# Kernel optimization log

Measured on AMD Instinct MI355X. Metric: run time of the kernel, lower is better.

The kernel has to match this reference:

```python
import jax, jax.numpy as jnp
import numpy as np

B, T, D = 64, 64, 64
E, HA, HB, OUT = 128, 128, 128, 1
SHORT = 2


def _rn(k, shape, scale=0.05):
    return jax.random.normal(k, shape, dtype=jnp.float32) * scale


def setup_inputs() -> dict:
    key = jax.random.key(0)
    ks = jax.random.split(key, 18)
    return {
        "x": jax.random.normal(ks[0], (B, T, D), dtype=jnp.float32),
        "W_emb": _rn(ks[1], (E, D)), "b_emb": _rn(ks[2], (E,)),
        "Wi_a": _rn(ks[3], (3 * HA, E)), "Wh_a": _rn(ks[4], (3 * HA, HA)),
        "bi_a": _rn(ks[5], (3 * HA,)), "bh_a": _rn(ks[6], (3 * HA,)),
        "Wi_b": _rn(ks[7], (3 * HB, E)), "Wh_b": _rn(ks[8], (3 * HB, HB)),
        "bi_b": _rn(ks[9], (3 * HB,)), "bh_b": _rn(ks[10], (3 * HB,)),
        "Wa": _rn(ks[11], (1, HA)), "ba": _rn(ks[12], (1,)),
        "Wb": _rn(ks[13], (E, HB)), "bb": _rn(ks[14], (E,)),
        "Wo": _rn(ks[15], (OUT, E)), "bo": _rn(ks[16], (OUT,)),
        "short": SHORT,
    }


def _gru_cell(x, h, Wi, Wh, bi, bh):
    # PyTorch GRU cell: gates ordered (r, z, n)
    gi = x @ Wi.T + bi
    gh = h @ Wh.T + bh
    ir, iz, in_ = jnp.split(gi, 3, axis=-1)
    hr, hz, hn = jnp.split(gh, 3, axis=-1)
    r = jax.nn.sigmoid(ir + hr)
    z = jax.nn.sigmoid(iz + hz)
    n = jnp.tanh(in_ + r * hn)
    return (1.0 - z) * n + z * h


def _forward(x, W_emb, b_emb, Wi_a, Wh_a, bi_a, bh_a, Wi_b, Wh_b, bi_b, bh_b,
             Wa, ba, Wb, bb, Wo, bo, short):
    Bn, Tn = x.shape[0], x.shape[1]
    temp = jnp.transpose(x, (1, 0, 2))            # [T, B, D]
    emb = temp @ W_emb.T + b_emb                  # [T, B, E]
    P = Tn - 1                                    # prefix p handles att_timesteps t = p+1
    S = Tn - 1                                    # max reversed-prefix length
    p_idx = jnp.arange(P)
    h0a = jnp.zeros((P, Bn, Wh_a.shape[1]), x.dtype)
    h0b = jnp.zeros((P, Bn, Wh_b.shape[1]), x.dtype)

    # All prefixes at once: for prefix p, reversed input at step s is emb[p - s].
    def step(carry, s):
        ha, hb = carry
        j = jnp.clip(p_idx - s, 0, Tn - 1)        # [P]
        e_in = emb[j]                             # [P, B, E]
        x_in = temp[j]                            # [P, B, D]
        na = _gru_cell(e_in, ha, Wi_a, Wh_a, bi_a, bh_a)
        nb = _gru_cell(e_in, hb, Wi_b, Wh_b, bi_b, bh_b)
        valid = (p_idx >= s)[:, None, None]
        ha = jnp.where(valid, na, ha)
        hb = jnp.where(valid, nb, hb)
        return (ha, hb), (ha, hb, e_in, x_in)

    _, (Ha, Hb, Eg, Xg) = jax.lax.scan(step, (h0a, h0b), jnp.arange(S))
    Ha = 0.5 * Ha                                 # reverse_h_a * 0.5, [S, P, B, HA]
    Hb = 0.5 * Hb                                 # reverse_h_b * 0.5, [S, P, B, HB]

    mask = p_idx[None, :] >= jnp.arange(S)[:, None]   # [S, P] valid scan steps
    preA = jnp.einsum('spbh,h->spb', Ha, Wa[0]) + ba[0]
    preA = jnp.where(mask[:, :, None], preA, -jnp.inf)
    alpha = jax.nn.softmax(preA, axis=0)              # softmax over prefix positions
    beta = jnp.tanh(jnp.einsum('spbh,eh->spbe', Hb, Wb) + bb)  # [S, P, B, E]

    # context: c[p] = sum_s alpha * beta * emb[p-s]  (softmax is order-invariant)
    c = jnp.einsum('spb,spbe->pbe', alpha, beta * Eg)          # [P, B, E]
    pred = c @ Wo.T + bo                                        # [P, B, 1]

    # interpretability weights: e = (beta * w_out) @ W_emb, f = alpha*e*x, g = mean over prefix
    e_chain = jnp.einsum('spbe,ed->spbd', beta * Wo[0], W_emb)  # [S, P, B, D]
    f = alpha[..., None] * e_chain * Xg
    g = jnp.sum(f, axis=0) / (p_idx[:, None, None] + 1.0)       # mean over t = p+1 steps

    pred = jnp.transpose(pred[short + 1:], (1, 0, 2))           # [B, T-2-short, 1]
    weight = jnp.transpose(g[short + 1:], (1, 0, 2))            # [B, T-2-short, D]
    return pred, weight


def reference(x, W_emb, b_emb, Wi_a, Wh_a, bi_a, bh_a, Wi_b, Wh_b, bi_b, bh_b,
              Wa, ba, Wb, bb, Wo, bo, short):
    return _forward(x, W_emb, b_emb, Wi_a, Wh_a, bi_a, bh_a, Wi_b, Wh_b, bi_b,
                    bh_b, Wa, ba, Wb, bb, Wo, bo, short)
```

## Files before the change

### kernel.cpp

```cpp
#include <hip/hip_runtime.h>
#include <hip/hip_bf16.h>
#include <math.h>

#define B_ 64
#define T_ 64
#define D_ 64
#define PMIN 3
#define NPOUT 60
#define NCHUNK 4

#define LOG2E     1.4426950408889634f
#define TWOLOG2E  2.8853900817779268f

typedef __hip_bfloat16 bf16;
typedef __attribute__((ext_vector_type(4))) short s16x4;
typedef __attribute__((ext_vector_type(8))) short s16x8;
typedef __attribute__((ext_vector_type(4))) float f32x4;

#define OFF_EMB   0
#define OFF_WIC2  524288
#define OFF_XT    622592
#define OFF_GIPK  884736
#define OFF_WPK   2457600
#define OFF_BPPK  2506752
#define OFF_WMPK  2514944
#define OFF_WALPK 2519040
#define OFF_FLAG  2520064

__device__ __forceinline__ float bf2f(unsigned short u) {
    union { float f; unsigned u32; } x; x.u32 = ((unsigned)u) << 16; return x.f;
}
__device__ __forceinline__ unsigned short f2bf(float f) {
    union { float f; unsigned u; } x; x.f = f;
    unsigned r = x.u + 0x7FFFu + ((x.u >> 16) & 1u);
    return (unsigned short)(r >> 16);
}
__device__ __forceinline__ float LDF(const void* p, int i, int flag) {
    return flag ? ((const float*)p)[i] : bf2f(((const unsigned short*)p)[i]);
}
__device__ __forceinline__ float sig2(float xneg) {
    return __builtin_amdgcn_rcpf(1.f + __builtin_exp2f(xneg));
}
__device__ __forceinline__ float tanh2(float x2) {
    return 1.f - 2.f * __builtin_amdgcn_rcpf(1.f + __builtin_exp2f(x2));
}
__device__ __forceinline__ int kpi(int s) {
    return (s & ~31) | ((s & 1) << 4) | ((s & 31) >> 1);
}

__global__ void detect_dtype(const unsigned short* xr, int* flag)
{
    int tid = threadIdx.x;
    int bad = 0;
    for (int i = tid; i < 4096; i += 256) {
        int ex = (xr[i] >> 7) & 0xFF;
        if (ex >= 140) bad++;
    }
    __shared__ int s[256];
    s[tid] = bad;
    __syncthreads();
    for (int st = 128; st > 0; st >>= 1) {
        if (tid < st) s[tid] += s[tid + st];
        __syncthreads();
    }
    if (tid == 0) *flag = (s[0] > 4) ? 1 : 0;
}

__global__ void prep_all(const void* p_x, const void* p_wemb,
                         const void* p_wia, const void* p_wib,
                         const void* p_wha, const void* p_whb,
                         const void* p_wa, const void* p_wb, const void* p_wo,
                         float* ws, const int* flagp)
{
    const int flag = *flagp;
    int id = blockIdx.x * 256 + threadIdx.x;
    if (id < 98304) {
        float v = (id < 49152) ? LDF(p_wia, id, flag)
                               : LDF(p_wib, id - 49152, flag);
        ws[OFF_WIC2 + id] = v;
    } else if (id < 360448) {
        int id5 = id - 98304;
        int b = id5 & 63, d = (id5 >> 6) & 63, t = id5 >> 12;
        ws[OFF_XT + id5] = LDF(p_x, (b * 64 + t) * 64 + d, flag);
    } else if (id < 458752) {
        unsigned short* wpk = (unsigned short*)(ws + OFF_WPK);
        int id3 = id - 360448;
        int w = id3 / 12288, r1 = id3 % 12288;
        int nt = r1 / 2048, r2 = r1 % 2048;
        int kt = r2 / 512, r3 = r2 % 512;
        int lane = r3 >> 3, j = r3 & 7;
        int cell = w >> 2, wv = w & 3;
        int gate = nt >> 1, tt = nt & 1;
        int g = gate * 128 + wv * 32 + tt * 16 + (lane & 15);
        int k = kpi(kt * 32 + (lane >> 4) * 8 + j);
        float sc = (gate < 2) ? -LOG2E : TWOLOG2E;
        wpk[id3] = f2bf(sc * LDF(cell ? p_whb : p_wha, g * 128 + k, flag));
    } else if (id < 475136) {
        unsigned short* bpk = (unsigned short*)(ws + OFF_BPPK);
        int id4 = id - 458752;
        int w = id4 / 2048, r = id4 % 2048;
        int kt = r / 512, lane = (r % 512) >> 3, j = r & 7;
        int e = w * 16 + (lane & 15);
        int k = kpi(kt * 32 + (lane >> 4) * 8 + j);
        bpk[id4] = f2bf(LOG2E * LDF(p_wb, e * 128 + k, flag));
    } else if (id < 483328) {
        unsigned short* wmk = (unsigned short*)(ws + OFF_WMPK);
        int id6 = id - 475136;
        int nt = id6 / 2048, r = id6 % 2048;
        int kt = r / 512, lane = (r % 512) >> 3, j = r & 7;
        int d = nt * 16 + (lane & 15);
        int e = kt * 32 + (lane >> 4) * 8 + j;
        wmk[id6] = f2bf(LDF(p_wo, e, flag) * LDF(p_wemb, e * 64 + d, flag));
    } else {
        unsigned short* alk = (unsigned short*)(ws + OFF_WALPK);
        int id7 = id - 483328;
        int kt = id7 / 512, lane = (id7 % 512) >> 3, j = id7 & 7;
        int k = kpi(kt * 32 + (lane >> 4) * 8 + j);
        alk[id7] = ((lane & 15) == 0) ? f2bf(0.5f * LOG2E * LDF(p_wa, k, flag))
                                      : (unsigned short)0;
    }
}

__global__ void prep_gi(float* ws, const void* p_x, const void* p_wemb,
                        const void* p_bemb, const void* p_bia, const void* p_bha,
                        const void* p_bib, const void* p_bhb, const int* flagp)
{
    const int flag = *flagp;
    unsigned short* gipk = (unsigned short*)(ws + OFF_GIPK);
    int t = blockIdx.x >> 3;
    int chunk = blockIdx.x & 7;
    int b0 = chunk * 8;
    int tid = threadIdx.x;
    __shared__ __align__(16) float sX[8][64];
    __shared__ __align__(16) float sWe[128][64];
    __shared__ __align__(16) float semT2[8][132];
    __shared__ __align__(16) unsigned short stg[6144];

    for (int i = tid; i < 512; i += 256) {
        int r = i >> 6, d = i & 63;
        sX[r][d] = LDF(p_x, ((b0 + r) * 64 + t) * 64 + d, flag);
    }
    for (int i = tid; i < 8192; i += 256)
        sWe[i >> 6][i & 63] = LDF(p_wemb, i, flag);
    __syncthreads();

    #pragma unroll
    for (int q = 0; q < 4; q++) {
        int o = tid + q * 256;
        int e = o & 127, r = o >> 7;
        float acc = LDF(p_bemb, e, flag);
        #pragma unroll
        for (int d = 0; d < 64; d += 4) {
            f32x4 xv = *(const f32x4*)&sX[r][d];
            f32x4 wv = *(const f32x4*)&sWe[e][d];
            acc += xv[0]*wv[0] + xv[1]*wv[1] + xv[2]*wv[2] + xv[3]*wv[3];
        }
        semT2[r][e] = acc;
        ws[OFF_EMB + (size_t)((t * 64 + b0 + r) * 128) + e] = acc;
    }
    __syncthreads();

    float acc3[3][8];
    #pragma unroll
    for (int g3 = 0; g3 < 3; g3++)
        #pragma unroll
        for (int r = 0; r < 8; r++) acc3[g3][r] = 0.f;
    const float* w2 = ws + OFF_WIC2;
    #pragma unroll 2
    for (int e0 = 0; e0 < 128; e0 += 4) {
        f32x4 wv0 = *(const f32x4*)(w2 + (size_t)(tid      ) * 128 + e0);
        f32x4 wv1 = *(const f32x4*)(w2 + (size_t)(tid + 256) * 128 + e0);
        f32x4 wv2 = *(const f32x4*)(w2 + (size_t)(tid + 512) * 128 + e0);
        f32x4 h[8];
        #pragma unroll
        for (int r = 0; r < 8; r++) h[r] = *(const f32x4*)&semT2[r][e0];
        #pragma unroll
        for (int r = 0; r < 8; r++)
            #pragma unroll
            for (int c = 0; c < 4; c++) {
                acc3[0][r] += wv0[c] * h[r][c];
                acc3[1][r] += wv1[c] * h[r][c];
                acc3[2][r] += wv2[c] * h[r][c];
            }
    }
    #pragma unroll
    for (int g3 = 0; g3 < 3; g3++) {
        int g = tid + g3 * 256;
        int cellg = g / 384, gr = g % 384;
        int gate = gr / 128, kh = gr % 128;
        int wvp = kh / 32, tt2 = (kh % 32) / 16, l15p = kh % 16;
        int wq = cellg * 4 + wvp;
        float bias = LDF(cellg ? p_bib : p_bia, gr, flag);
        if (gate < 2) bias += LDF(cellg ? p_bhb : p_bha, gr, flag);
        float sc = (gate < 2) ? -LOG2E : TWOLOG2E;
        #pragma unroll
        for (int r = 0; r < 8; r++) {
            float v = sc * (acc3[g3][r] + bias);
            int lane2 = (r >> 2) * 16 + l15p;
            int slot = gate * 8 + tt2 * 4 + (r & 3);
            stg[(wq * 32 + lane2) * 24 + slot] = f2bf(v);
        }
    }
    __syncthreads();
    const uint4* s4 = (const uint4*)stg;
    const int c16 = chunk >> 1, rhalf = chunk & 1;
    uint4* d4 = (uint4*)(gipk + (size_t)(t * 4 + c16) * 12288);
    for (int i = tid; i < 768; i += 256) {
        int wq = i / 96, rem = i % 96;
        d4[wq * 192 + rhalf * 96 + rem] = s4[i];
    }
}


__launch_bounds__(512, 1)
__global__ void chain_kernel(const float* ws, void* outv, const int* flagp,
                             const void* p_bha, const void* p_bhb,
                             const void* p_bb, const void* p_ba,
                             const void* p_bo, const void* p_wo)
{
    const int p = PMIN + (NPOUT - 1) - (int)blockIdx.x / NCHUNK;
    const int chunk = (int)blockIdx.x % NCHUNK;
    const int tid = threadIdx.x;
    const int lane = tid & 63;
    const int w = tid >> 6;
    const int cell = w >> 2;
    const int wv = w & 3;
    const int l15 = lane & 15;
    const int quad = lane >> 4;

    __shared__ __align__(16) short hbf[2][2][16][136];
    __shared__ __align__(16) short betbf[2][16][136];
    __shared__ __align__(16) short sWm[4][4][64][8];
    __shared__ float weLds[2][16];

    const unsigned short* gipk = (const unsigned short*)(ws + OFF_GIPK);
    const unsigned short* wpk  = (const unsigned short*)(ws + OFF_WPK);
    const unsigned short* bpk  = (const unsigned short*)(ws + OFF_BPPK);
    const unsigned short* alk  = (const unsigned short*)(ws + OFF_WALPK);
    const int flag = *flagp;

    {
        const int* s2 = (const int*)(ws + OFF_WMPK);
        int* d2 = (int*)&sWm[0][0][0][0];
        for (int i = tid; i < 4096; i += 512) d2[i] = s2[i];
        int* hz = (int*)&hbf[0][0][0][0];
        for (int i = tid; i < 4352; i += 512) hz[i] = 0;
        int* bz = (int*)&betbf[0][0][0];
        for (int i = tid; i < 2176; i += 512) bz[i] = 0;
    }

    s16x8 wB[6][4];
    #pragma unroll
    for (int nt = 0; nt < 6; nt++)
        #pragma unroll
        for (int kt = 0; kt < 4; kt++)
            wB[nt][kt] = *(const s16x8*)(wpk + (((w * 6 + nt) * 4 + kt) * 64 + lane) * 8);
    s16x8 bBp[4], wAl[4];
    #pragma unroll
    for (int kt = 0; kt < 4; kt++)
        bBp[kt] = *(const s16x8*)(bpk + ((w * 4 + kt) * 64 + lane) * 8);
    if (w == 7) {
        #pragma unroll
        for (int kt = 0; kt < 4; kt++)
            wAl[kt] = *(const s16x8*)(alk + (kt * 64 + lane) * 8);
    }

    const float bhnS0 = TWOLOG2E *
        LDF(cell ? p_bhb : p_bha, 256 + wv * 32 + l15, flag);
    const float bhnS1 = TWOLOG2E *
        LDF(cell ? p_bhb : p_bha, 256 + wv * 32 + 16 + l15, flag);
    const float bbE2 = TWOLOG2E * LDF(p_bb, w * 16 + l15, flag);
    const float bafS = LOG2E * LDF(p_ba, 0, flag);
    const float bof  = LDF(p_bo, 0, flag);

    float h_old[8];
    #pragma unroll
    for (int i = 0; i < 8; i++) h_old[i] = 0.f;
    float accR[9];
    #pragma unroll
    for (int i = 0; i < 9; i++) accR[i] = 0.f;

    f32x4 xvP = (f32x4){0.f,0.f,0.f,0.f};
    f32x4 em0P = (f32x4){0.f,0.f,0.f,0.f};
    f32x4 em1P = (f32x4){0.f,0.f,0.f,0.f};

    auto phaseC = [&](int dbufP) {
        if (w < 4) {
            f32x4 ec = (f32x4){0.f,0.f,0.f,0.f};
            #pragma unroll
            for (int kt = 0; kt < 4; kt++) {
                s16x8 a = *(const s16x8*)&betbf[dbufP][l15][kt * 32 + quad * 8];
                s16x8 bw = *(const s16x8*)&sWm[w][kt][lane][0];
                ec = __builtin_amdgcn_mfma_f32_16x16x32_bf16(a, bw, ec, 0, 0, 0);
            }
            #pragma unroll
            for (int reg = 0; reg < 4; reg++) {
                float we = weLds[dbufP][quad * 4 + reg];
                accR[4 + reg] += we;
                accR[reg] += we * ec[reg] * xvP[reg];
            }
        } else {
            const int row = quad * 4 + (w - 4);
            float we = weLds[dbufP][row];
            accR[8] += we;
            const short* bp2 = &betbf[dbufP][row][l15 * 8];
            s16x4 blo = *(const s16x4*)bp2;
            s16x4 bhi = *(const s16x4*)(bp2 + 4);
            #pragma unroll
            for (int v = 0; v < 4; v++)
                accR[v] += we * bf2f((unsigned short)blo[v]) * em0P[v];
            #pragma unroll
            for (int v = 0; v < 4; v++)
                accR[4 + v] += we * bf2f((unsigned short)bhi[v]) * em1P[v];
        }
    };

    __syncthreads();

    for (int it = 0; it <= p + 1; it++) {
        const int j = p - it;
        const int jp = j + 1;
        const bool doGru = (j >= 0);
        const int cur = it & 1;
        const int nxt = cur ^ 1;
        const int dbuf = it & 1;

        s16x8 giv[3];
        if (doGru) {
            const unsigned short* gp0 =
                gipk + ((((size_t)j * 4 + chunk) * 8 + w) * 64 + lane) * 24;
            giv[0] = *(const s16x8*)(gp0);
            giv[1] = *(const s16x8*)(gp0 + 8);
            giv[2] = *(const s16x8*)(gp0 + 16);
        }

        if (it > 1) phaseC(dbuf ^ 1);

        if (it > 0) {
            if (w < 4) {
                xvP = *(const f32x4*)(ws + OFF_XT + ((size_t)jp * 64 + w * 16 + l15) * 64
                                      + chunk * 16 + quad * 4);
            } else {
                const int row = quad * 4 + (w - 4);
                const float* ep = ws + OFF_EMB
                                  + ((size_t)jp * 64 + chunk * 16 + row) * 128 + l15 * 8;
                em0P = *(const f32x4*)ep;
                em1P = *(const f32x4*)(ep + 4);
            }
        }

        f32x4 Cg[6], Cbp, Cal;
        #pragma unroll
        for (int nt = 0; nt < 6; nt++) Cg[nt] = (f32x4){0.f,0.f,0.f,0.f};
        Cbp = (f32x4){0.f,0.f,0.f,0.f};
        Cal = (f32x4){0.f,0.f,0.f,0.f};

        #pragma unroll
        for (int kt = 0; kt < 4; kt++) {
            s16x8 aB = *(const s16x8*)&hbf[cur][1][l15][kt * 32 + quad * 8];
            s16x8 aA;
            if (cell == 0 || w == 7) aA = *(const s16x8*)&hbf[cur][0][l15][kt * 32 + quad * 8];
            else aA = aB;
            s16x8 aOwn = cell ? aB : aA;
            #pragma unroll
            for (int nt = 0; nt < 6; nt++)
                Cg[nt] = __builtin_amdgcn_mfma_f32_16x16x32_bf16(aOwn, wB[nt][kt], Cg[nt], 0, 0, 0);
            Cbp = __builtin_amdgcn_mfma_f32_16x16x32_bf16(aB, bBp[kt], Cbp, 0, 0, 0);
            if (w == 7)
                Cal = __builtin_amdgcn_mfma_f32_16x16x32_bf16(aA, wAl[kt], Cal, 0, 0, 0);
        }

        if (w == 7 && l15 == 0) {
            #pragma unroll
            for (int reg = 0; reg < 4; reg++)
                weLds[dbuf][quad * 4 + reg] =
                    __builtin_exp2f(fminf(Cal[reg] + bafS, 86.f));
        }
        if (doGru) {
            #pragma unroll
            for (int reg = 0; reg < 4; reg++) {
                float rr0 = sig2(bf2f((unsigned short)giv[0][reg]) + Cg[0][reg]);
                float zz0 = sig2(bf2f((unsigned short)giv[1][reg]) + Cg[2][reg]);
                float nn0 = tanh2(bf2f((unsigned short)giv[2][reg])
                                  + rr0 * (Cg[4][reg] + bhnS0));
                float h0 = (1.f - zz0) * nn0 + zz0 * h_old[reg];
                h_old[reg] = h0;
                float rr1 = sig2(bf2f((unsigned short)giv[0][4 + reg]) + Cg[1][reg]);
                float zz1 = sig2(bf2f((unsigned short)giv[1][4 + reg]) + Cg[3][reg]);
                float nn1 = tanh2(bf2f((unsigned short)giv[2][4 + reg])
                                  + rr1 * (Cg[5][reg] + bhnS1));
                float h1 = (1.f - zz1) * nn1 + zz1 * h_old[4 + reg];
                h_old[4 + reg] = h1;
                unsigned pk;
                asm("v_cvt_pk_bf16_f32 %0, %1, %2" : "=v"(pk) : "v"(h0), "v"(h1));
                *(unsigned*)&hbf[nxt][cell][quad * 4 + reg][wv * 32 + l15 * 2] = pk;
            }
        }
        {
            #pragma unroll
            for (int reg = 0; reg < 4; reg++) {
                float bv = tanh2(Cbp[reg] + bbE2);
                betbf[dbuf][quad * 4 + reg][w * 16 + l15] = (short)f2bf(bv);
            }
        }

        __syncthreads();
    }

    phaseC((p + 1) & 1);

    if (w >= 4) {
        const int row = quad * 4 + (w - 4);
        float wo8[8];
        if (flag) {
            const float* wp = (const float*)p_wo + l15 * 8;
            #pragma unroll
            for (int v = 0; v < 8; v++) wo8[v] = wp[v];
        } else {
            const unsigned short* wp = (const unsigned short*)p_wo + l15 * 8;
            #pragma unroll
            for (int v = 0; v < 8; v++) wo8[v] = bf2f(wp[v]);
        }
        float part = 0.f;
        #pragma unroll
        for (int v = 0; v < 8; v++) part += accR[v] * wo8[v];
        part += __shfl_xor(part, 1);
        part += __shfl_xor(part, 2);
        part += __shfl_xor(part, 4);
        part += __shfl_xor(part, 8);
        if (l15 == 0) {
            int bglob = chunk * 16 + row;
            float pr = part / accR[8] + bof;
            size_t oi = (size_t)bglob * NPOUT + (p - PMIN);
            if (flag) ((float*)outv)[oi] = pr;
            else      ((bf16*)outv)[oi] = __float2bfloat16(pr);
        }
    } else {
        const float invt = 1.f / (float)(p + 1);
        #pragma unroll
        for (int reg = 0; reg < 4; reg++) {
            int row = quad * 4 + reg;
            int bglob = chunk * 16 + row;
            float gv = accR[reg] / accR[4 + reg] * invt;
            size_t oi = (size_t)B_ * NPOUT
                      + ((size_t)bglob * NPOUT + (p - PMIN)) * 64 + w * 16 + l15;
            if (flag) ((float*)outv)[oi] = gv;
            else      ((bf16*)outv)[oi] = __float2bfloat16(gv);
        }
    }
}

extern "C" void kernel_launch(void* const* d_in, const int* in_sizes, int n_in,
                              void* d_out, int out_size, void* d_ws, size_t ws_size,
                              hipStream_t stream)
{
    float* ws = (float*)d_ws;
    int* flagp = (int*)(ws + OFF_FLAG);

    hipLaunchKernelGGL(detect_dtype, dim3(1), dim3(256), 0, stream,
                       (const unsigned short*)d_in[0], flagp);
    hipLaunchKernelGGL(prep_all, dim3(1896), dim3(256), 0, stream,
                       d_in[0], d_in[1], d_in[3], d_in[7], d_in[4], d_in[8],
                       d_in[11], d_in[13], d_in[15], ws, flagp);
    hipLaunchKernelGGL(prep_gi, dim3(512), dim3(256), 0, stream,
                       ws, d_in[0], d_in[1], d_in[2], d_in[5], d_in[6],
                       d_in[9], d_in[10], flagp);
    hipLaunchKernelGGL(chain_kernel, dim3(NPOUT * NCHUNK), dim3(512), 0, stream,
                       ws, d_out, flagp,
                       d_in[6], d_in[10], d_in[14], d_in[12], d_in[16], d_in[15]);
}
```

Before: 314.3 us.

## Fuse dtype detection, prep, and chain kernels into one persistent kernel with grid barrier

Merges the four launches (dtype detect, weight packing, input-gate precompute, recurrent chain) into one 240-workgroup kernel. Each workgroup detects the dtype itself, does a strided share of the packing and gate tasks (16 batch rows per task, reading Wi directly from the inputs rather than a staged fp32 copy), then meets the others at an atomic-counter grid barrier before running the chain. This removes launch overheads and intermediate kernel boundaries. The barrier relies on all 240 workgroups being co-resident, and LDS use grows because the prep buffers share the kernel with the chain buffers.

Result: slower. 367.8 us (+17.0%).

```diff
diff --git a/kernel.cpp b/kernel.cpp
--- a/kernel.cpp
+++ b/kernel.cpp
@@ -8,6 +8,7 @@
 #define PMIN 3
 #define NPOUT 60
 #define NCHUNK 4
+#define NWG (NPOUT * NCHUNK)
 
 #define LOG2E     1.4426950408889634f
 #define TWOLOG2E  2.8853900817779268f
@@ -18,14 +19,13 @@
 typedef __attribute__((ext_vector_type(4))) float f32x4;
 
 #define OFF_EMB   0
-#define OFF_WIC2  524288
 #define OFF_XT    622592
 #define OFF_GIPK  884736
 #define OFF_WPK   2457600
 #define OFF_BPPK  2506752
 #define OFF_WMPK  2514944
 #define OFF_WALPK 2519040
-#define OFF_FLAG  2520064
+#define OFF_CNT   2520064
 
 __device__ __forceinline__ float bf2f(unsigned short u) {
     union { float f; unsigned u32; } x; x.u32 = ((unsigned)u) << 16; return x.f;
@@ -38,6 +38,12 @@
 __device__ __forceinline__ float LDF(const void* p, int i, int flag) {
     return flag ? ((const float*)p)[i] : bf2f(((const unsigned short*)p)[i]);
 }
+__device__ __forceinline__ f32x4 LDF4(const void* p, int i, int flag) {
+    if (flag) return *(const f32x4*)((const float*)p + i);
+    s16x4 v = *(const s16x4*)((const unsigned short*)p + i);
+    return (f32x4){bf2f((unsigned short)v[0]), bf2f((unsigned short)v[1]),
+                   bf2f((unsigned short)v[2]), bf2f((unsigned short)v[3])};
+}
 __device__ __forceinline__ float sig2(float xneg) {
     return __builtin_amdgcn_rcpf(1.f + __builtin_exp2f(xneg));
 }
@@ -48,179 +54,189 @@
     return (s & ~31) | ((s & 1) << 4) | ((s & 31) >> 1);
 }
 
-__global__ void detect_dtype(const unsigned short* xr, int* flag)
+
+__launch_bounds__(512, 1)
+__global__ void fused_kernel(const void* p_x, const void* p_wemb, const void* p_bemb,
+                             const void* p_wia, const void* p_wha, const void* p_bia,
+                             const void* p_bha, const void* p_wib, const void* p_whb,
+                             const void* p_bib, const void* p_bhb, const void* p_wa,
+                             const void* p_ba, const void* p_wb, const void* p_bb,
+                             const void* p_wo, const void* p_bo,
+                             float* ws, void* outv)
 {
-    int tid = threadIdx.x;
-    int bad = 0;
-    for (int i = tid; i < 4096; i += 256) {
-        int ex = (xr[i] >> 7) & 0xFF;
-        if (ex >= 140) bad++;
-    }
-    __shared__ int s[256];
-    s[tid] = bad;
+    const int wgid = (int)blockIdx.x;
+    const int tid = threadIdx.x;
+
+    __shared__ __align__(16) float sWe[128][64];
+    __shared__ __align__(16) float sX[16][64];
+    __shared__ __align__(16) float semT2[16][132];
+    __shared__ __align__(16) unsigned short stg[12288];
+    __shared__ __align__(16) short hbf[2][2][16][136];
+    __shared__ __align__(16) short betbf[2][16][136];
+    __shared__ __align__(16) short sWm[4][4][64][8];
+    __shared__ float weLds[2][16];
+
+    unsigned short* gipk = (unsigned short*)(ws + OFF_GIPK);
+
+    int flag;
+    {
+        const unsigned short* xr = (const unsigned short*)p_x;
+        int bad = 0;
+        for (int i = tid; i < 4096; i += 512) {
+            int ex = (xr[i] >> 7) & 0xFF;
+            if (ex >= 140) bad++;
+        }
+        int* s = (int*)stg;
+        s[tid] = bad;
+        __syncthreads();
+        for (int st = 256; st > 0; st >>= 1) {
+            if (tid < st) s[tid] += s[tid + st];
+            __syncthreads();
+        }
+        flag = (s[0] > 4) ? 1 : 0;
+        __syncthreads();
+    }
+
+    for (int id = wgid * 512 + tid; id < 387072; id += NWG * 512) {
+        if (id < 262144) {
+            int b = id & 63, d = (id >> 6) & 63, t = id >> 12;
+            ws[OFF_XT + id] = LDF(p_x, (b * 64 + t) * 64 + d, flag);
+        } else if (id < 360448) {
+            unsigned short* wpk = (unsigned short*)(ws + OFF_WPK);
+            int id3 = id - 262144;
+            int w = id3 / 12288, r1 = id3 % 12288;
+            int nt = r1 / 2048, r2 = r1 % 2048;
+            int kt = r2 / 512, r3 = r2 % 512;
+            int lane = r3 >> 3, j = r3 & 7;
+            int cell = w >> 2, wv = w & 3;
+            int gate = nt >> 1, tt = nt & 1;
+            int g = gate * 128 + wv * 32 + tt * 16 + (lane & 15);
+            int k = kpi(kt * 32 + (lane >> 4) * 8 + j);
+            float sc = (gate < 2) ? -LOG2E : TWOLOG2E;
+            wpk[id3] = f2bf(sc * LDF(cell ? p_whb : p_wha, g * 128 + k, flag));
+        } else if (id < 376832) {
+            unsigned short* bpk = (unsigned short*)(ws + OFF_BPPK);
+            int id4 = id - 360448;
+            int w = id4 / 2048, r = id4 % 2048;
+            int kt = r / 512, lane = (r % 512) >> 3, j = r & 7;
+            int e = w * 16 + (lane & 15);
+            int k = kpi(kt * 32 + (lane >> 4) * 8 + j);
+            bpk[id4] = f2bf(LOG2E * LDF(p_wb, e * 128 + k, flag));
+        } else if (id < 385024) {
+            unsigned short* wmk = (unsigned short*)(ws + OFF_WMPK);
+            int id6 = id - 376832;
+            int nt = id6 / 2048, r = id6 % 2048;
+            int kt = r / 512, lane = (r % 512) >> 3, j = r & 7;
+            int d = nt * 16 + (lane & 15);
+            int e = kt * 32 + (lane >> 4) * 8 + j;
+            wmk[id6] = f2bf(LDF(p_wo, e, flag) * LDF(p_wemb, e * 64 + d, flag));
+        } else {
+            unsigned short* alk = (unsigned short*)(ws + OFF_WALPK);
+            int id7 = id - 385024;
+            int kt = id7 / 512, lane = (id7 % 512) >> 3, j = id7 & 7;
+            int k = kpi(kt * 32 + (lane >> 4) * 8 + j);
+            alk[id7] = ((lane & 15) == 0) ? f2bf(0.5f * LOG2E * LDF(p_wa, k, flag))
+                                          : (unsigned short)0;
+        }
+    }
+
+    for (int i = tid; i < 2048; i += 512) {
+        int e = i >> 4, d4 = (i & 15) << 2;
+        *(f32x4*)&sWe[e][d4] = LDF4(p_wemb, e * 64 + d4, flag);
+    }
+
+    for (int task = wgid; task < 256; task += NWG) {
+        const int t = task >> 2, c16 = task & 3, b0 = c16 * 16;
+        __syncthreads();
+        for (int i = tid; i < 1024; i += 512) {
+            int r = i >> 6, d = i & 63;
+            sX[r][d] = LDF(p_x, ((b0 + r) * 64 + t) * 64 + d, flag);
+        }
+        __syncthreads();
+
+        #pragma unroll
+        for (int q = 0; q < 4; q++) {
+            int o = tid + q * 512;
+            int e = o & 127, r = o >> 7;
+            float acc = LDF(p_bemb, e, flag);
+            #pragma unroll
+            for (int d = 0; d < 64; d += 4) {
+                f32x4 xv = *(const f32x4*)&sX[r][d];
+                f32x4 wv = *(const f32x4*)&sWe[e][d];
+                acc += xv[0]*wv[0] + xv[1]*wv[1] + xv[2]*wv[2] + xv[3]*wv[3];
+            }
+            semT2[r][e] = acc;
+            ws[OFF_EMB + (size_t)((t * 64 + b0 + r) * 128) + e] = acc;
+        }
+        __syncthreads();
+
+        const int q8 = tid & 255, half = tid >> 8;
+        float acc3[3][8];
+        #pragma unroll
+        for (int g3 = 0; g3 < 3; g3++)
+            #pragma unroll
+            for (int r = 0; r < 8; r++) acc3[g3][r] = 0.f;
+        const void* pW0; const void* pW1; const void* pW2;
+        int row0, row1, row2;
+        {
+            int g0 = q8;           pW0 = p_wia;                          row0 = g0;
+            int g1 = q8 + 256;     pW1 = (g1 >= 384) ? p_wib : p_wia;    row1 = (g1 >= 384) ? g1 - 384 : g1;
+            int g2 = q8 + 512;     pW2 = p_wib;                          row2 = g2 - 384;
+        }
+        #pragma unroll 2
+        for (int e0 = 0; e0 < 128; e0 += 4) {
+            f32x4 wv0 = LDF4(pW0, row0 * 128 + e0, flag);
+            f32x4 wv1 = LDF4(pW1, row1 * 128 + e0, flag);
+            f32x4 wv2 = LDF4(pW2, row2 * 128 + e0, flag);
+            f32x4 h[8];
+            #pragma unroll
+            for (int r = 0; r < 8; r++) h[r] = *(const f32x4*)&semT2[half * 8 + r][e0];
+            #pragma unroll
+            for (int r = 0; r < 8; r++)
+                #pragma unroll
+                for (int c = 0; c < 4; c++) {
+                    acc3[0][r] += wv0[c] * h[r][c];
+                    acc3[1][r] += wv1[c] * h[r][c];
+                    acc3[2][r] += wv2[c] * h[r][c];
+                }
+        }
+        #pragma unroll
+        for (int g3 = 0; g3 < 3; g3++) {
+            int g = q8 + g3 * 256;
+            int cellg = g / 384, gr = g % 384;
+            int gate = gr / 128, kh = gr % 128;
+            int wvp = kh / 32, tt2 = (kh % 32) / 16, l15p = kh % 16;
+            int wq = cellg * 4 + wvp;
+            float bias = LDF(cellg ? p_bib : p_bia, gr, flag);
+            if (gate < 2) bias += LDF(cellg ? p_bhb : p_bha, gr, flag);
+            float sc = (gate < 2) ? -LOG2E : TWOLOG2E;
+            #pragma unroll
+            for (int rr = 0; rr < 8; rr++) {
+                int r = half * 8 + rr;
+                float v = sc * (acc3[g3][rr] + bias);
+                int lane2 = (r >> 2) * 16 + l15p;
+                int slot = gate * 8 + tt2 * 4 + (rr & 3);
+                stg[(wq * 64 + lane2) * 24 + slot] = f2bf(v);
+            }
+        }
+        __syncthreads();
+        const uint4* s4 = (const uint4*)stg;
+        uint4* d4 = (uint4*)(gipk + (size_t)(t * 4 + c16) * 12288);
+        for (int i = tid; i < 1536; i += 512) d4[i] = s4[i];
+    }
+
     __syncthreads();
-    for (int st = 128; st > 0; st >>= 1) {
-        if (tid < st) s[tid] += s[tid + st];
-        __syncthreads();
-    }
-    if (tid == 0) *flag = (s[0] > 4) ? 1 : 0;
-}
-
-__global__ void prep_all(const void* p_x, const void* p_wemb,
-                         const void* p_wia, const void* p_wib,
-                         const void* p_wha, const void* p_whb,
-                         const void* p_wa, const void* p_wb, const void* p_wo,
-                         float* ws, const int* flagp)
-{
-    const int flag = *flagp;
-    int id = blockIdx.x * 256 + threadIdx.x;
-    if (id < 98304) {
-        float v = (id < 49152) ? LDF(p_wia, id, flag)
-                               : LDF(p_wib, id - 49152, flag);
-        ws[OFF_WIC2 + id] = v;
-    } else if (id < 360448) {
-        int id5 = id - 98304;
-        int b = id5 & 63, d = (id5 >> 6) & 63, t = id5 >> 12;
-        ws[OFF_XT + id5] = LDF(p_x, (b * 64 + t) * 64 + d, flag);
-    } else if (id < 458752) {
-        unsigned short* wpk = (unsigned short*)(ws + OFF_WPK);
-        int id3 = id - 360448;
-        int w = id3 / 12288, r1 = id3 % 12288;
-        int nt = r1 / 2048, r2 = r1 % 2048;
-        int kt = r2 / 512, r3 = r2 % 512;
-        int lane = r3 >> 3, j = r3 & 7;
-        int cell = w >> 2, wv = w & 3;
-        int gate = nt >> 1, tt = nt & 1;
-        int g = gate * 128 + wv * 32 + tt * 16 + (lane & 15);
-        int k = kpi(kt * 32 + (lane >> 4) * 8 + j);
-        float sc = (gate < 2) ? -LOG2E : TWOLOG2E;
-        wpk[id3] = f2bf(sc * LDF(cell ? p_whb : p_wha, g * 128 + k, flag));
-    } else if (id < 475136) {
-        unsigned short* bpk = (unsigned short*)(ws + OFF_BPPK);
-        int id4 = id - 458752;
-        int w = id4 / 2048, r = id4 % 2048;
-        int kt = r / 512, lane = (r % 512) >> 3, j = r & 7;
-        int e = w * 16 + (lane & 15);
-        int k = kpi(kt * 32 + (lane >> 4) * 8 + j);
-        bpk[id4] = f2bf(LOG2E * LDF(p_wb, e * 128 + k, flag));
-    } else if (id < 483328) {
-        unsigned short* wmk = (unsigned short*)(ws + OFF_WMPK);
-        int id6 = id - 475136;
-        int nt = id6 / 2048, r = id6 % 2048;
-        int kt = r / 512, lane = (r % 512) >> 3, j = r & 7;
-        int d = nt * 16 + (lane & 15);
-        int e = kt * 32 + (lane >> 4) * 8 + j;
-        wmk[id6] = f2bf(LDF(p_wo, e, flag) * LDF(p_wemb, e * 64 + d, flag));
-    } else {
-        unsigned short* alk = (unsigned short*)(ws + OFF_WALPK);
-        int id7 = id - 483328;
-        int kt = id7 / 512, lane = (id7 % 512) >> 3, j = id7 & 7;
-        int k = kpi(kt * 32 + (lane >> 4) * 8 + j);
-        alk[id7] = ((lane & 15) == 0) ? f2bf(0.5f * LOG2E * LDF(p_wa, k, flag))
-                                      : (unsigned short)0;
-    }
-}
-
-__global__ void prep_gi(float* ws, const void* p_x, const void* p_wemb,
-                        const void* p_bemb, const void* p_bia, const void* p_bha,
-                        const void* p_bib, const void* p_bhb, const int* flagp)
-{
-    const int flag = *flagp;
-    unsigned short* gipk = (unsigned short*)(ws + OFF_GIPK);
-    int t = blockIdx.x >> 3;
-    int chunk = blockIdx.x & 7;
-    int b0 = chunk * 8;
-    int tid = threadIdx.x;
-    __shared__ __align__(16) float sX[8][64];
-    __shared__ __align__(16) float sWe[128][64];
-    __shared__ __align__(16) float semT2[8][132];
-    __shared__ __align__(16) unsigned short stg[6144];
-
-    for (int i = tid; i < 512; i += 256) {
-        int r = i >> 6, d = i & 63;
-        sX[r][d] = LDF(p_x, ((b0 + r) * 64 + t) * 64 + d, flag);
-    }
-    for (int i = tid; i < 8192; i += 256)
-        sWe[i >> 6][i & 63] = LDF(p_wemb, i, flag);
+    if (tid == 0) {
+        int* gcnt = (int*)(ws + OFF_CNT);
+        __threadfence();
+        atomicAdd(gcnt, 1);
+        while (atomicAdd(gcnt, 0) < NWG) {}
+        __threadfence();
+    }
     __syncthreads();
 
-    #pragma unroll
-    for (int q = 0; q < 4; q++) {
-        int o = tid + q * 256;
-        int e = o & 127, r = o >> 7;
-        float acc = LDF(p_bemb, e, flag);
-        #pragma unroll
-        for (int d = 0; d < 64; d += 4) {
-            f32x4 xv = *(const f32x4*)&sX[r][d];
-            f32x4 wv = *(const f32x4*)&sWe[e][d];
-            acc += xv[0]*wv[0] + xv[1]*wv[1] + xv[2]*wv[2] + xv[3]*wv[3];
-        }
-        semT2[r][e] = acc;
-        ws[OFF_EMB + (size_t)((t * 64 + b0 + r) * 128) + e] = acc;
-    }
-    __syncthreads();
-
-    float acc3[3][8];
-    #pragma unroll
-    for (int g3 = 0; g3 < 3; g3++)
-        #pragma unroll
-        for (int r = 0; r < 8; r++) acc3[g3][r] = 0.f;
-    const float* w2 = ws + OFF_WIC2;
-    #pragma unroll 2
-    for (int e0 = 0; e0 < 128; e0 += 4) {
-        f32x4 wv0 = *(const f32x4*)(w2 + (size_t)(tid      ) * 128 + e0);
-        f32x4 wv1 = *(const f32x4*)(w2 + (size_t)(tid + 256) * 128 + e0);
-        f32x4 wv2 = *(const f32x4*)(w2 + (size_t)(tid + 512) * 128 + e0);
-        f32x4 h[8];
-        #pragma unroll
-        for (int r = 0; r < 8; r++) h[r] = *(const f32x4*)&semT2[r][e0];
-        #pragma unroll
-        for (int r = 0; r < 8; r++)
-            #pragma unroll
-            for (int c = 0; c < 4; c++) {
-                acc3[0][r] += wv0[c] * h[r][c];
-                acc3[1][r] += wv1[c] * h[r][c];
-                acc3[2][r] += wv2[c] * h[r][c];
-            }
-    }
-    #pragma unroll
-    for (int g3 = 0; g3 < 3; g3++) {
-        int g = tid + g3 * 256;
-        int cellg = g / 384, gr = g % 384;
-        int gate = gr / 128, kh = gr % 128;
-        int wvp = kh / 32, tt2 = (kh % 32) / 16, l15p = kh % 16;
-        int wq = cellg * 4 + wvp;
-        float bias = LDF(cellg ? p_bib : p_bia, gr, flag);
-        if (gate < 2) bias += LDF(cellg ? p_bhb : p_bha, gr, flag);
-        float sc = (gate < 2) ? -LOG2E : TWOLOG2E;
-        #pragma unroll
-        for (int r = 0; r < 8; r++) {
-            float v = sc * (acc3[g3][r] + bias);
-            int lane2 = (r >> 2) * 16 + l15p;
-            int slot = gate * 8 + tt2 * 4 + (r & 3);
-            stg[(wq * 32 + lane2) * 24 + slot] = f2bf(v);
-        }
-    }
-    __syncthreads();
-    const uint4* s4 = (const uint4*)stg;
-    const int c16 = chunk >> 1, rhalf = chunk & 1;
-    uint4* d4 = (uint4*)(gipk + (size_t)(t * 4 + c16) * 12288);
-    for (int i = tid; i < 768; i += 256) {
-        int wq = i / 96, rem = i % 96;
-        d4[wq * 192 + rhalf * 96 + rem] = s4[i];
-    }
-}
-
-
-__launch_bounds__(512, 1)
-__global__ void chain_kernel(const float* ws, void* outv, const int* flagp,
-                             const void* p_bha, const void* p_bhb,
-                             const void* p_bb, const void* p_ba,
-                             const void* p_bo, const void* p_wo)
-{
-    const int p = PMIN + (NPOUT - 1) - (int)blockIdx.x / NCHUNK;
-    const int chunk = (int)blockIdx.x % NCHUNK;
-    const int tid = threadIdx.x;
+    const int p = PMIN + (NPOUT - 1) - wgid / NCHUNK;
+    const int chunk = wgid % NCHUNK;
     const int lane = tid & 63;
     const int w = tid >> 6;
     const int cell = w >> 2;
@@ -228,16 +244,9 @@
     const int l15 = lane & 15;
     const int quad = lane >> 4;
 
-    __shared__ __align__(16) short hbf[2][2][16][136];
-    __shared__ __align__(16) short betbf[2][16][136];
-    __shared__ __align__(16) short sWm[4][4][64][8];
-    __shared__ float weLds[2][16];
-
-    const unsigned short* gipk = (const unsigned short*)(ws + OFF_GIPK);
     const unsigned short* wpk  = (const unsigned short*)(ws + OFF_WPK);
     const unsigned short* bpk  = (const unsigned short*)(ws + OFF_BPPK);
     const unsigned short* alk  = (const unsigned short*)(ws + OFF_WALPK);
-    const int flag = *flagp;
 
     {
         const int* s2 = (const int*)(ws + OFF_WMPK);
@@ -455,17 +464,10 @@
                               hipStream_t stream)
 {
     float* ws = (float*)d_ws;
-    int* flagp = (int*)(ws + OFF_FLAG);
-
-    hipLaunchKernelGGL(detect_dtype, dim3(1), dim3(256), 0, stream,
-                       (const unsigned short*)d_in[0], flagp);
-    hipLaunchKernelGGL(prep_all, dim3(1896), dim3(256), 0, stream,
-                       d_in[0], d_in[1], d_in[3], d_in[7], d_in[4], d_in[8],
-                       d_in[11], d_in[13], d_in[15], ws, flagp);
-    hipLaunchKernelGGL(prep_gi, dim3(512), dim3(256), 0, stream,
-                       ws, d_in[0], d_in[1], d_in[2], d_in[5], d_in[6],
-                       d_in[9], d_in[10], flagp);
-    hipLaunchKernelGGL(chain_kernel, dim3(NPOUT * NCHUNK), dim3(512), 0, stream,
-                       ws, d_out, flagp,
-                       d_in[6], d_in[10], d_in[14], d_in[12], d_in[16], d_in[15]);
-}
+    hipMemsetAsync((void*)(ws + OFF_CNT), 0, sizeof(int), stream);
+    hipLaunchKernelGGL(fused_kernel, dim3(NWG), dim3(512), 0, stream,
+                       d_in[0], d_in[1], d_in[2], d_in[3], d_in[4], d_in[5],
+                       d_in[6], d_in[7], d_in[8], d_in[9], d_in[10], d_in[11],
+                       d_in[12], d_in[13], d_in[14], d_in[15], d_in[16],
+                       ws, d_out);
+}
```
